# Optimization experiments

Measured on AMD Instinct MI355X. Metric: run time of the kernel, lower is better.

Reference implementation:

```python
import jax, jax.numpy as jnp
import numpy as np

LMAX = 3
NBASIS = 10
MAX_RADIUS = 10.0
NUM_GRAPHS = 1024
N_NODES = 50000
Z_DIM = 16
SH_DIM = (LMAX + 1) ** 2  # 16
SMOOTH_FINITE_C = 1.14136  # e3nn normalization constant for smooth_finite basis


def spherical_harmonics_l3(vec):
    """e3nn real spherical harmonics, lmax=3, normalize=True, normalization='component'.
    vec: [N,3] -> [N,16]."""
    r = jnp.linalg.norm(vec, axis=-1, keepdims=True)
    u = vec / r
    x, y, z = u[..., 0], u[..., 1], u[..., 2]
    one = jnp.ones_like(x)
    s3, s5, s7, s15 = np.sqrt(3.0), np.sqrt(5.0), np.sqrt(7.0), np.sqrt(15.0)
    x2, y2, z2 = x * x, y * y, z * z
    x2z2 = x2 + z2
    # l = 2 (e3nn generated polynomials, component normalization)
    sh2_0 = s15 * x * z
    sh2_1 = s15 * x * y
    sh2_2 = s5 * (y2 - 0.5 * x2z2)
    sh2_3 = s15 * y * z
    sh2_4 = (s15 / 2.0) * (z2 - x2)
    # l = 3
    c42_6 = np.sqrt(42.0) / 6.0
    c168_8 = np.sqrt(168.0) / 8.0
    sh3_0 = c42_6 * (sh2_0 * z + sh2_4 * x)
    sh3_1 = s7 * sh2_0 * y
    sh3_2 = c168_8 * (4.0 * y2 - x2z2) * x
    sh3_3 = (s7 / 2.0) * y * (2.0 * y2 - 3.0 * x2z2)
    sh3_4 = c168_8 * z * (4.0 * y2 - x2z2)
    sh3_5 = s7 * sh2_4 * y
    sh3_6 = c42_6 * (sh2_4 * z - sh2_0 * x)
    return jnp.stack([
        one,
        s3 * x, s3 * y, s3 * z,
        sh2_0, sh2_1, sh2_2, sh2_3, sh2_4,
        sh3_0, sh3_1, sh3_2, sh3_3, sh3_4, sh3_5, sh3_6,
    ], axis=-1)


def soft_one_hot_smooth_finite(d):
    """e3nn soft_one_hot_linspace(basis='smooth_finite', cutoff=True). d: [N] -> [N, NBASIS]."""
    values = jnp.linspace(0.0, MAX_RADIUS, NBASIS + 2)[1:-1]  # interior points
    step = MAX_RADIUS / (NBASIS + 1)
    diff = (d[:, None] - values) / step

    def soft_unit_step(u):
        safe = jnp.where(u > 0.0, u, 1.0)
        return jnp.where(u > 0.0, jnp.exp(-1.0 / safe), 0.0)

    c = SMOOTH_FINITE_C * np.exp(2.0)
    return c * soft_unit_step(diff + 1.0) * soft_unit_step(1.0 - diff)


def setup_inputs() -> dict:
    key = jax.random.key(0)
    k1, k2, k3 = jax.random.split(key, 3)
    x = jax.random.uniform(k1, (N_NODES, Z_DIM), dtype=jnp.float32)
    pos = jax.random.normal(k2, (N_NODES, 3), dtype=jnp.float32)
    batch = jnp.sort(jax.random.randint(k3, (N_NODES,), 0, NUM_GRAPHS, dtype=jnp.int64))
    return {"x": x, "pos": pos, "batch": batch}


def reference(x, pos, batch):
    edge_vec = pos
    edge_length = jnp.linalg.norm(edge_vec, axis=1)
    # radial embedding, scaled by sqrt(number_of_basis)
    basis = soft_one_hot_smooth_finite(edge_length) * np.sqrt(NBASIS)  # [N, B]
    sh = spherical_harmonics_l3(edge_vec)  # [N, 16]
    # FullTensorProduct(Zx0e, sh) then FullTensorProduct(., Bx0e):
    # scalar x irrep paths reduce to exact elementwise products (component norm),
    # with e3nn layout per l-block: [z, b, m] flattened, blocks concatenated over l.
    n = x.shape[0]
    sh_slices = [(0, 1), (1, 4), (4, 9), (9, 16)]  # l = 0..3
    blocks = []
    for lo, hi in sh_slices:
        blk = jnp.einsum('nz,nb,nm->nzbm', x, basis, sh[:, lo:hi])
        blocks.append(blk.reshape(n, -1))
    feats = jnp.concatenate(blocks, axis=-1)  # [N, Z*B*16]
    # scatter mean over graphs
    seg_sum = jax.ops.segment_sum(feats, batch, num_segments=NUM_GRAPHS)
    cnt = jax.ops.segment_sum(jnp.ones((n, 1), dtype=feats.dtype), batch, num_segments=NUM_GRAPHS)
    return seg_sum / jnp.maximum(cnt, 1.0)
```

## Files before the change

### kernel.cpp

```cpp
#include <hip/hip_runtime.h>
#include <cmath>

#define NGRAPHS 1024
#define ZDIM 16
#define NB 10
#define SHD 16
#define FEAT 2560
#define CHUNK 128
#define CPAD (CHUNK + 4)
#define WIN 1536

__global__ __launch_bounds__(256) void yfe_kernel(
    const float* __restrict__ xin,
    const float* __restrict__ pos,
    const int* __restrict__ batch,
    float* __restrict__ out,
    int n_nodes)
{
    const int g = blockIdx.x;
    const int tid = threadIdx.x;
    const int n = n_nodes;

    __shared__ int s_red[12];
    __shared__ __align__(16) float s_xT[ZDIM][CPAD];
    __shared__ __align__(16) float s_shA[SHD][CPAD];
    __shared__ __align__(16) float s_shB[SHD][CPAD];
    __shared__ __align__(16) unsigned int s_ib4[CHUNK / 4];
    __shared__ __align__(16) float s_out[FEAT];

    int start, end;
    bool window_ok = (n >= WIN);
    if (window_ok) {
        const int ctr = (int)(((long long)(2 * g + 1) * n) >> 11);
        int p0 = ctr - WIN / 2;
        if (p0 < 0) p0 = 0;
        if (p0 > n - WIN) p0 = n - WIN;
        int vals[6];
#pragma unroll
        for (int k = 0; k < 6; ++k) vals[k] = batch[p0 + tid + k * 256];
        int wA = 0, wB = 0;
#pragma unroll
        for (int k = 0; k < 6; ++k) {
            wA += __popcll(__ballot(vals[k] < g));
            wB += __popcll(__ballot(vals[k] < g + 1));
        }
        if ((tid & 63) == 0) {
            s_red[tid >> 6]       = wA;
            s_red[4 + (tid >> 6)] = wB;
        }
        if (tid == 0)   s_red[8] = vals[0];
        if (tid == 255) s_red[9] = vals[5];
        __syncthreads();
        const int KA = s_red[0] + s_red[1] + s_red[2] + s_red[3];
        const int KB = s_red[4] + s_red[5] + s_red[6] + s_red[7];
        start = p0 + KA;
        end   = p0 + KB;
        const bool left_ok  = (p0 == 0) || (s_red[8] < g);
        const bool right_ok = (p0 + WIN == n) || (s_red[9] >= g + 1);
        window_ok = left_ok && right_ok;
        __syncthreads();
    }
    if (!window_ok) {
        {
            const int pos1 = (int)(((long long)tid * n) >> 8);
            const int v = batch[pos1];
            const unsigned long long balA = __ballot(v < g);
            const unsigned long long balB = __ballot(v < g + 1);
            if ((tid & 63) == 0) {
                s_red[tid >> 6]       = __popcll(balA);
                s_red[4 + (tid >> 6)] = __popcll(balB);
            }
        }
        __syncthreads();
        const int KA = s_red[0] + s_red[1] + s_red[2] + s_red[3];
        const int KB = s_red[4] + s_red[5] + s_red[6] + s_red[7];
        const int loA = (KA == 0) ? 0 : (int)(((long long)(KA - 1) * n) >> 8) + 1;
        const int hiA = (KA == 256) ? n : (int)(((long long)KA * n) >> 8);
        const int loB = (KB == 0) ? 0 : (int)(((long long)(KB - 1) * n) >> 8) + 1;
        const int hiB = (KB == 256) ? n : (int)(((long long)KB * n) >> 8);
        __syncthreads();
        const int pA = loA + tid;
        const int pB = loB + tid;
        const int prA = (pA < hiA) ? (batch[pA] < g) : 0;
        const int prB = (pB < hiB) ? (batch[pB] < g + 1) : 0;
        const unsigned long long balA = __ballot(prA);
        const unsigned long long balB = __ballot(prB);
        if ((tid & 63) == 0) {
            s_red[tid >> 6]       = __popcll(balA);
            s_red[4 + (tid >> 6)] = __popcll(balB);
        }
        __syncthreads();
        start = loA + s_red[0] + s_red[1] + s_red[2] + s_red[3];
        end   = loB + s_red[4] + s_red[5] + s_red[6] + s_red[7];
        __syncthreads();
    }
    const int cnt = end - start;

    const int zi  = tid >> 4;
    const int shi = tid & 15;
    const int l   = (shi >= 9) ? 3 : (shi >= 4) ? 2 : (shi >= 1) ? 1 : 0;
    const int m   = shi - l * l;
    const int w   = 2 * l + 1;
    const int off = (l == 0) ? 0 : (l == 1) ? 160 : (l == 2) ? 640 : 1440;
    const int fbase = off + zi * 10 * w + m;

    float acc[NB];
#pragma unroll
    for (int b = 0; b < NB; ++b) acc[b] = 0.0f;

    const float CB = (float)(1.14136 * 7.389056098930650 * 3.1622776601683795);

    for (int nb0 = start; nb0 < end; nb0 += CHUNK) {
        const int nrem  = min(CHUNK, end - nb0);
        const int nrem4 = (nrem + 3) & ~3;
        __syncthreads();
        for (int idx = tid; idx < nrem * 4; idx += 256) {
            const int c = idx >> 2, zq = (idx & 3) * 4;
            const float4 xv = *(const float4*)(xin + (size_t)(nb0 + c) * ZDIM + zq);
            s_xT[zq + 0][c] = xv.x;
            s_xT[zq + 1][c] = xv.y;
            s_xT[zq + 2][c] = xv.z;
            s_xT[zq + 3][c] = xv.w;
        }
        if (tid < nrem) {
            const int node = nb0 + tid;
            const float px = pos[node * 3 + 0];
            const float py = pos[node * 3 + 1];
            const float pz = pos[node * 3 + 2];
            const float r2 = px * px + py * py + pz * pz;
            const float rinv = rsqrtf(r2);
            const float X = px * rinv, Y = py * rinv, Z = pz * rinv;
            const float x2 = X * X, y2 = Y * Y, z2 = Z * Z;
            const float x2z2 = x2 + z2;
            const float s3  = 1.7320508075688772f;
            const float s5  = 2.2360679774997896f;
            const float s7  = 2.6457513110645907f;
            const float s15 = 3.8729833462074170f;
            const float c42_6  = 1.0801234497346435f;
            const float c168_8 = 1.6201851746019651f;
            const float sh2_0 = s15 * X * Z;
            const float sh2_1 = s15 * X * Y;
            const float sh2_2 = s5 * (y2 - 0.5f * x2z2);
            const float sh2_3 = s15 * Y * Z;
            const float sh2_4 = 0.5f * s15 * (z2 - x2);
            float sh[SHD];
            sh[0]  = 1.0f;
            sh[1]  = s3 * X;
            sh[2]  = s3 * Y;
            sh[3]  = s3 * Z;
            sh[4]  = sh2_0;
            sh[5]  = sh2_1;
            sh[6]  = sh2_2;
            sh[7]  = sh2_3;
            sh[8]  = sh2_4;
            sh[9]  = c42_6 * (sh2_0 * Z + sh2_4 * X);
            sh[10] = s7 * sh2_0 * Y;
            sh[11] = c168_8 * (4.0f * y2 - x2z2) * X;
            sh[12] = 0.5f * s7 * Y * (2.0f * y2 - 3.0f * x2z2);
            sh[13] = c168_8 * Z * (4.0f * y2 - x2z2);
            sh[14] = s7 * sh2_4 * Y;
            sh[15] = c42_6 * (sh2_4 * Z - sh2_0 * X);
            const float d = r2 * rinv;
            const float t = d * 1.1f;
            int ib = (int)floorf(t) - 1;
            ib = min(max(ib, 0), 8);
            float bvA = 0.0f, bvB = 0.0f;
            {
                const float u1 = t - (float)ib, u2 = (float)(ib + 2) - t;
                if (u1 > 0.0f && u2 > 0.0f) bvA = CB * __expf(-1.0f / u1 - 1.0f / u2);
                const float v1 = t - (float)(ib + 1), v2 = (float)(ib + 3) - t;
                if (v1 > 0.0f && v2 > 0.0f) bvB = CB * __expf(-1.0f / v1 - 1.0f / v2);
            }
#pragma unroll
            for (int k = 0; k < SHD; ++k) {
                s_shA[k][tid] = sh[k] * bvA;
                s_shB[k][tid] = sh[k] * bvB;
            }
            ((unsigned char*)s_ib4)[tid] = (unsigned char)ib;
        } else if (tid < nrem4) {
#pragma unroll
            for (int k = 0; k < SHD; ++k) {
                s_xT[k][tid] = 0.0f; s_shA[k][tid] = 0.0f; s_shB[k][tid] = 0.0f;
            }
            ((unsigned char*)s_ib4)[tid] = 0;
        }
        __syncthreads();

#define ACC1(XQ, SA, SB, IB_)                                                    \
        {                                                                        \
            const float xq_ = (XQ);                                              \
            switch (IB_) {                                                       \
                case 0: acc[0] += xq_ * (SA); acc[1] += xq_ * (SB); break;       \
                case 1: acc[1] += xq_ * (SA); acc[2] += xq_ * (SB); break;       \
                case 2: acc[2] += xq_ * (SA); acc[3] += xq_ * (SB); break;       \
                case 3: acc[3] += xq_ * (SA); acc[4] += xq_ * (SB); break;       \
                case 4: acc[4] += xq_ * (SA); acc[5] += xq_ * (SB); break;       \
                case 5: acc[5] += xq_ * (SA); acc[6] += xq_ * (SB); break;       \
                case 6: acc[6] += xq_ * (SA); acc[7] += xq_ * (SB); break;       \
                case 7: acc[7] += xq_ * (SA); acc[8] += xq_ * (SB); break;       \
                default: acc[8] += xq_ * (SA); acc[9] += xq_ * (SB); break;      \
            }                                                                    \
        }

#pragma unroll 2
        for (int c = 0; c < nrem4; c += 4) {
            const float4 xv = *(const float4*)&s_xT[zi][c];
            const float4 sA = *(const float4*)&s_shA[shi][c];
            const float4 sB = *(const float4*)&s_shB[shi][c];
            const unsigned int ibw =
                (unsigned int)__builtin_amdgcn_readfirstlane((int)s_ib4[c >> 2]);
            ACC1(xv.x, sA.x, sB.x, (int)(ibw & 255u));
            ACC1(xv.y, sA.y, sB.y, (int)((ibw >> 8) & 255u));
            ACC1(xv.z, sA.z, sB.z, (int)((ibw >> 16) & 255u));
            ACC1(xv.w, sA.w, sB.w, (int)(ibw >> 24));
        }
#undef ACC1
    }

    const float scale = 1.0f / (float)max(cnt, 1);
#pragma unroll
    for (int b = 0; b < NB; ++b) s_out[fbase + b * w] = acc[b] * scale;
    __syncthreads();
    float4* og4 = (float4*)(out + (size_t)g * FEAT);
    const float4* so4 = (const float4*)s_out;
    for (int i = tid; i < FEAT / 4; i += 256) og4[i] = so4[i];
}

extern "C" void kernel_launch(void* const* d_in, const int* in_sizes, int n_in,
                              void* d_out, int out_size, void* d_ws, size_t ws_size,
                              hipStream_t stream) {
    const float* x   = (const float*)d_in[0];
    const float* pos = (const float*)d_in[1];
    const int* batch = (const int*)d_in[2];
    float* out = (float*)d_out;
    const int n_nodes = in_sizes[2];

    hipLaunchKernelGGL(yfe_kernel, dim3(NGRAPHS), dim3(256), 0, stream,
                       x, pos, batch, out, n_nodes);
}
```

Baseline: 70.25 us.

## Bucket nodes by radial bin in shared memory to remove per-node switch

Each chunk's nodes are now sorted into nine buckets by radial basis index, using ballot and popcount to compute ranks and per-wave counts. Each bucket is padded to a multiple of four, so the inner accumulation loop uses fixed accumulator indices per bucket instead of a per-node switch. Chunk size drops to 96 and each chunk now clears all shared buffers, which adds an extra barrier, zeroing traffic, and up to 36 padding columns of wasted work. The x loads are now done per thread as four float4 loads instead of the earlier cooperative transpose.

```diff
diff --git a/kernel.cpp b/kernel.cpp
--- a/kernel.cpp
+++ b/kernel.cpp
@@ -6,8 +6,8 @@
 #define NB 10
 #define SHD 16
 #define FEAT 2560
-#define CHUNK 128
-#define CPAD (CHUNK + 4)
+#define CHUNK 96
+#define CSTRIDE 132
 #define WIN 1536
 
 __global__ __launch_bounds__(256) void yfe_kernel(
@@ -22,10 +22,10 @@
     const int n = n_nodes;
 
     __shared__ int s_red[12];
-    __shared__ __align__(16) float s_xT[ZDIM][CPAD];
-    __shared__ __align__(16) float s_shA[SHD][CPAD];
-    __shared__ __align__(16) float s_shB[SHD][CPAD];
-    __shared__ __align__(16) unsigned int s_ib4[CHUNK / 4];
+    __shared__ int s_cnt[2][9];
+    __shared__ __align__(16) float s_xT[ZDIM][CSTRIDE];
+    __shared__ __align__(16) float s_shA[SHD][CSTRIDE];
+    __shared__ __align__(16) float s_shB[SHD][CSTRIDE];
     __shared__ __align__(16) float s_out[FEAT];
 
     int start, end;
@@ -111,19 +111,28 @@
     const float CB = (float)(1.14136 * 7.389056098930650 * 3.1622776601683795);
 
     for (int nb0 = start; nb0 < end; nb0 += CHUNK) {
-        const int nrem  = min(CHUNK, end - nb0);
-        const int nrem4 = (nrem + 3) & ~3;
-        __syncthreads();
-        for (int idx = tid; idx < nrem * 4; idx += 256) {
-            const int c = idx >> 2, zq = (idx & 3) * 4;
-            const float4 xv = *(const float4*)(xin + (size_t)(nb0 + c) * ZDIM + zq);
-            s_xT[zq + 0][c] = xv.x;
-            s_xT[zq + 1][c] = xv.y;
-            s_xT[zq + 2][c] = xv.z;
-            s_xT[zq + 3][c] = xv.w;
-        }
+        const int nrem = min(CHUNK, end - nb0);
+        __syncthreads();
+
+        {
+            const float4 z4 = make_float4(0.f, 0.f, 0.f, 0.f);
+            float4* zx = (float4*)s_xT;
+            float4* za = (float4*)s_shA;
+            float4* zb = (float4*)s_shB;
+            for (int i = tid; i < (ZDIM * CSTRIDE) / 4; i += 256) {
+                zx[i] = z4; za[i] = z4; zb[i] = z4;
+            }
+        }
+
+        int   my_ib = 9;
+        int   my_rank = 0;
+        float4 xr0, xr1, xr2, xr3;
+        float sh[SHD];
+        float bvA = 0.0f, bvB = 0.0f;
         if (tid < nrem) {
             const int node = nb0 + tid;
+            const float4* xp = (const float4*)(xin + (size_t)node * ZDIM);
+            xr0 = xp[0]; xr1 = xp[1]; xr2 = xp[2]; xr3 = xp[3];
             const float px = pos[node * 3 + 0];
             const float py = pos[node * 3 + 1];
             const float pz = pos[node * 3 + 2];
@@ -143,7 +152,6 @@
             const float sh2_2 = s5 * (y2 - 0.5f * x2z2);
             const float sh2_3 = s15 * Y * Z;
             const float sh2_4 = 0.5f * s15 * (z2 - x2);
-            float sh[SHD];
             sh[0]  = 1.0f;
             sh[1]  = s3 * X;
             sh[2]  = s3 * Y;
@@ -164,57 +172,69 @@
             const float t = d * 1.1f;
             int ib = (int)floorf(t) - 1;
             ib = min(max(ib, 0), 8);
-            float bvA = 0.0f, bvB = 0.0f;
             {
                 const float u1 = t - (float)ib, u2 = (float)(ib + 2) - t;
                 if (u1 > 0.0f && u2 > 0.0f) bvA = CB * __expf(-1.0f / u1 - 1.0f / u2);
                 const float v1 = t - (float)(ib + 1), v2 = (float)(ib + 3) - t;
                 if (v1 > 0.0f && v2 > 0.0f) bvB = CB * __expf(-1.0f / v1 - 1.0f / v2);
             }
+            my_ib = ib;
+        }
+        if (tid < 128) {
+            const unsigned long long lt = (1ull << (unsigned)(tid & 63)) - 1ull;
+#pragma unroll
+            for (int v = 0; v < 9; ++v) {
+                const unsigned long long bal = __ballot(my_ib == v);
+                if (my_ib == v) my_rank = __popcll(bal & lt);
+                if ((tid & 63) == 0) s_cnt[tid >> 6][v] = __popcll(bal);
+            }
+        }
+        __syncthreads();
+
+        int cum[10];
+        {
+            cum[0] = 0;
+#pragma unroll
+            for (int v = 0; v < 9; ++v)
+                cum[v + 1] = cum[v] + ((s_cnt[0][v] + s_cnt[1][v] + 3) & ~3);
+        }
+
+        if (tid < nrem) {
+            int dest = my_rank;
+            if (tid >= 64) dest += s_cnt[0][my_ib];
+#pragma unroll
+            for (int v = 0; v < 9; ++v) {
+                const int pv = (s_cnt[0][v] + s_cnt[1][v] + 3) & ~3;
+                dest += (v < my_ib) ? pv : 0;
+            }
 #pragma unroll
             for (int k = 0; k < SHD; ++k) {
-                s_shA[k][tid] = sh[k] * bvA;
-                s_shB[k][tid] = sh[k] * bvB;
-            }
-            ((unsigned char*)s_ib4)[tid] = (unsigned char)ib;
-        } else if (tid < nrem4) {
-#pragma unroll
-            for (int k = 0; k < SHD; ++k) {
-                s_xT[k][tid] = 0.0f; s_shA[k][tid] = 0.0f; s_shB[k][tid] = 0.0f;
-            }
-            ((unsigned char*)s_ib4)[tid] = 0;
-        }
-        __syncthreads();
-
-#define ACC1(XQ, SA, SB, IB_)                                                    \
-        {                                                                        \
-            const float xq_ = (XQ);                                              \
-            switch (IB_) {                                                       \
-                case 0: acc[0] += xq_ * (SA); acc[1] += xq_ * (SB); break;       \
-                case 1: acc[1] += xq_ * (SA); acc[2] += xq_ * (SB); break;       \
-                case 2: acc[2] += xq_ * (SA); acc[3] += xq_ * (SB); break;       \
-                case 3: acc[3] += xq_ * (SA); acc[4] += xq_ * (SB); break;       \
-                case 4: acc[4] += xq_ * (SA); acc[5] += xq_ * (SB); break;       \
-                case 5: acc[5] += xq_ * (SA); acc[6] += xq_ * (SB); break;       \
-                case 6: acc[6] += xq_ * (SA); acc[7] += xq_ * (SB); break;       \
-                case 7: acc[7] += xq_ * (SA); acc[8] += xq_ * (SB); break;       \
-                default: acc[8] += xq_ * (SA); acc[9] += xq_ * (SB); break;      \
-            }                                                                    \
-        }
-
-#pragma unroll 2
-        for (int c = 0; c < nrem4; c += 4) {
-            const float4 xv = *(const float4*)&s_xT[zi][c];
-            const float4 sA = *(const float4*)&s_shA[shi][c];
-            const float4 sB = *(const float4*)&s_shB[shi][c];
-            const unsigned int ibw =
-                (unsigned int)__builtin_amdgcn_readfirstlane((int)s_ib4[c >> 2]);
-            ACC1(xv.x, sA.x, sB.x, (int)(ibw & 255u));
-            ACC1(xv.y, sA.y, sB.y, (int)((ibw >> 8) & 255u));
-            ACC1(xv.z, sA.z, sB.z, (int)((ibw >> 16) & 255u));
-            ACC1(xv.w, sA.w, sB.w, (int)(ibw >> 24));
-        }
-#undef ACC1
+                s_shA[k][dest] = sh[k] * bvA;
+                s_shB[k][dest] = sh[k] * bvB;
+            }
+            s_xT[ 0][dest] = xr0.x; s_xT[ 1][dest] = xr0.y;
+            s_xT[ 2][dest] = xr0.z; s_xT[ 3][dest] = xr0.w;
+            s_xT[ 4][dest] = xr1.x; s_xT[ 5][dest] = xr1.y;
+            s_xT[ 6][dest] = xr1.z; s_xT[ 7][dest] = xr1.w;
+            s_xT[ 8][dest] = xr2.x; s_xT[ 9][dest] = xr2.y;
+            s_xT[10][dest] = xr2.z; s_xT[11][dest] = xr2.w;
+            s_xT[12][dest] = xr3.x; s_xT[13][dest] = xr3.y;
+            s_xT[14][dest] = xr3.z; s_xT[15][dest] = xr3.w;
+        }
+        __syncthreads();
+
+#pragma unroll
+        for (int v = 0; v < 9; ++v) {
+            for (int c = cum[v]; c < cum[v + 1]; c += 4) {
+                const float4 xv = *(const float4*)&s_xT[zi][c];
+                const float4 sA = *(const float4*)&s_shA[shi][c];
+                const float4 sB = *(const float4*)&s_shB[shi][c];
+                acc[v] = fmaf(xv.w, sA.w, fmaf(xv.z, sA.z,
+                         fmaf(xv.y, sA.y, fmaf(xv.x, sA.x, acc[v]))));
+                acc[v + 1] = fmaf(xv.w, sB.w, fmaf(xv.z, sB.z,
+                             fmaf(xv.y, sB.y, fmaf(xv.x, sB.x, acc[v + 1]))));
+            }
+        }
     }
 
     const float scale = 1.0f / (float)max(cnt, 1);
```

After: 65.74 us. 1.07x faster.
